# Kernel optimization log

Measured on AMD Instinct MI355X. Metric: run time of the kernel, lower is better.

Reference implementation:

```python
import jax, jax.numpy as jnp
import numpy as np

N = 50000      # nodes
E = 800000     # edges (before self-loops)
D = 128        # input_dim == hidden_dim
L = 3          # num_layers
EPS = 1e-5     # BatchNorm eps


def setup_inputs() -> dict:
    key = jax.random.key(0)
    k0, k1, k2 = jax.random.split(key, 3)
    x = jax.random.normal(k0, (N, D), dtype=jnp.float32)
    edge_index = jax.random.randint(k1, (2, E), 0, N, dtype=jnp.int32)
    # stacked per-layer params (layer 0 is input_dim->hidden, same shape since D==hidden)
    W = jax.random.normal(k2, (L, D, D), dtype=jnp.float32) / np.float32(np.sqrt(D))
    b = jnp.zeros((L, D), dtype=jnp.float32)
    gamma = jnp.ones((L, D), dtype=jnp.float32)
    beta = jnp.zeros((L, D), dtype=jnp.float32)
    return {"x": x, "edge_index": edge_index, "W": W, "b": b, "gamma": gamma, "beta": beta}


def reference(x, edge_index, W, b, gamma, beta):
    # --- GCN symmetric normalization with self-loops (PyG GCNConv default) ---
    loop = jnp.arange(N, dtype=edge_index.dtype)
    src = jnp.concatenate([edge_index[0], loop])      # [E+N]
    dst = jnp.concatenate([edge_index[1], loop])      # [E+N]
    deg = jax.ops.segment_sum(jnp.ones_like(dst, dtype=x.dtype), dst, num_segments=N)
    dinv = jax.lax.rsqrt(deg)                          # deg >= 1 due to self-loops
    norm = (dinv[src] * dinv[dst])[:, None]            # [E+N, 1]

    h = x
    for i in range(L):
        # GCNConv: aggregate norm * (h W)[src] into dst, then bias
        m = h @ W[i]                                   # [N, D]
        h = jax.ops.segment_sum(m[src] * norm, dst, num_segments=N) + b[i]
        # BatchNorm1d (training-mode batch statistics, biased variance)
        mu = jnp.mean(h, axis=0)
        var = jnp.var(h, axis=0)
        h = gamma[i] * (h - mu) * jax.lax.rsqrt(var + EPS) + beta[i]
        # ReLU; dropout is identity in eval mode
        h = jax.nn.relu(h)
    return h
```

## Files before the change

kernel.cpp:

```cpp
#include <hip/hip_runtime.h>
#include <hip/hip_bf16.h>

#define N_NODES 50000
#define N_EDGES 800000
#define DIM 128
#define BN_EPS 1e-5f
#define GATHER_BLOCKS (N_NODES / 4)
#define RED_BLOCKS 125
#define CAP 48

typedef __attribute__((ext_vector_type(8))) short short8;
typedef __attribute__((ext_vector_type(4))) float float4v;

__device__ __forceinline__ float bf16_bits_to_f32(unsigned short u) {
    union { unsigned int i; float f; } c;
    c.i = ((unsigned int)u) << 16;
    return c.f;
}

__device__ __forceinline__ float bf16_lo(unsigned int u) {
    union { unsigned int i; float f; } c;
    c.i = u << 16;
    return c.f;
}

__device__ __forceinline__ float bf16_hi(unsigned int u) {
    union { unsigned int i; float f; } c;
    c.i = u & 0xFFFF0000u;
    return c.f;
}

__device__ __forceinline__ unsigned short f32_to_bf16_bits(float f) {
    union { float f; unsigned int i; } c;
    c.f = f;
    unsigned int lsb = (c.i >> 16) & 1u;
    c.i += 0x7FFFu + lsb;
    return (unsigned short)(c.i >> 16);
}

__global__ __launch_bounds__(256) void sniff(const unsigned short* __restrict__ xu,
                                             float* __restrict__ mode) {
    __shared__ int cnt;
    if (threadIdx.x == 0) cnt = 0;
    __syncthreads();
    int ok = 0;
    for (int i = threadIdx.x; i < 512; i += 256) {
        unsigned e = (xu[i] >> 7) & 0xFFu;
        if (e >= 96u && e <= 159u) ok++;
    }
    atomicAdd(&cnt, ok);
    __syncthreads();
    if (threadIdx.x == 0) mode[0] = (cnt >= 480) ? 0.0f : 1.0f;
}

__global__ __launch_bounds__(256) void zero_buf(float* __restrict__ p, int n) {
    int i = blockIdx.x * blockDim.x + threadIdx.x;
    if (i < n) p[i] = 0.0f;
}

__global__ __launch_bounds__(256) void zero_int(int* __restrict__ p, int n) {
    int i = blockIdx.x * blockDim.x + threadIdx.x;
    if (i < n) p[i] = 0;
}

__global__ __launch_bounds__(256) void convert_params(
    const void* __restrict__ W, const void* __restrict__ b,
    const void* __restrict__ g, const void* __restrict__ be,
    const float* __restrict__ mode,
    unsigned short* __restrict__ Wt, float* __restrict__ pf32) {
    const bool mf32 = mode[0] > 0.5f;
    int i = blockIdx.x * blockDim.x + threadIdx.x;
    const int NW = 3 * DIM * DIM;
    if (i < NW) {
        int l = i >> 14;
        int rem = i & 16383;
        int k = rem >> 7;
        int n = rem & 127;
        unsigned short v = mf32 ? f32_to_bf16_bits(((const float*)W)[i])
                                : ((const unsigned short*)W)[i];
        Wt[(size_t)l * DIM * DIM + (size_t)n * DIM + k] = v;
    } else if (i < NW + 3 * 3 * DIM) {
        int p = i - NW;
        int which = p / 384;
        int r = p - which * 384;
        const void* srcp = (which == 0) ? b : (which == 1) ? g : be;
        float v = mf32 ? ((const float*)srcp)[r]
                       : bf16_bits_to_f32(((const unsigned short*)srcp)[r]);
        pf32[which * 384 + r] = v;
    }
}

__global__ __launch_bounds__(256) void fill_padded(
    const int* __restrict__ src, const int* __restrict__ dst,
    int* __restrict__ cnt, unsigned short* __restrict__ colu) {
    int e = blockIdx.x * blockDim.x + threadIdx.x;
    if (e >= N_EDGES) return;
    int s = src[e], d = dst[e];
    int pos = atomicAdd(&cnt[d], 1);
    if (pos < CAP) colu[(size_t)d * CAP + pos] = (unsigned short)s;
}

__global__ __launch_bounds__(256) void make_dinv(const int* __restrict__ cnt,
                                                 float* __restrict__ dinv) {
    int v = blockIdx.x * blockDim.x + threadIdx.x;
    if (v < N_NODES) dinv[v] = rsqrtf((float)cnt[v] + 1.0f);
}

__global__ __launch_bounds__(256) void gemm_scale(
    const void* hsrc, int kind, int b_bf16,
    const unsigned short* __restrict__ Wt,
    const float* __restrict__ dinv,
    const float* __restrict__ mode,
    const float* __restrict__ alpha, const float* __restrict__ delta,
    unsigned short* A, float* __restrict__ B, int write_b) {
    const int wave = threadIdx.x >> 6;
    const int lane = threadIdx.x & 63;
    const int quad = lane >> 4;
    const int nidx = lane & 15;
    const int row0 = blockIdx.x * 16;

    short8 afrag[4];
    if (kind == 0) {
        if (mode[0] > 0.5f) {
            const float* xf = (const float*)hsrc;
            #pragma unroll
            for (int kk = 0; kk < 4; ++kk) {
                const float4v* xr = (const float4v*)(xf + (size_t)(row0 + nidx) * DIM + kk * 32 + quad * 8);
                float4v p0 = xr[0], p1 = xr[1];
                #pragma unroll
                for (int j = 0; j < 4; ++j) {
                    afrag[kk][j]     = (short)f32_to_bf16_bits(p0[j]);
                    afrag[kk][4 + j] = (short)f32_to_bf16_bits(p1[j]);
                }
            }
        } else {
            const unsigned short* hu = (const unsigned short*)hsrc;
            #pragma unroll
            for (int kk = 0; kk < 4; ++kk)
                afrag[kk] = *(const short8*)(hu + (size_t)(row0 + nidx) * DIM + kk * 32 + quad * 8);
        }
    } else if (b_bf16) {
        const unsigned short* Bh = (const unsigned short*)hsrc;
        const float dv = dinv[row0 + nidx];
        #pragma unroll
        for (int kk = 0; kk < 4; ++kk) {
            short8 braw = *(const short8*)(Bh + (size_t)(row0 + nidx) * DIM + kk * 32 + quad * 8);
            const float* ap = alpha + kk * 32 + quad * 8;
            const float* dp = delta + kk * 32 + quad * 8;
            float4v A0 = *(const float4v*)ap, A1 = *(const float4v*)(ap + 4);
            float4v D0 = *(const float4v*)dp, D1 = *(const float4v*)(dp + 4);
            #pragma unroll
            for (int j = 0; j < 4; ++j) {
                float v0 = bf16_bits_to_f32((unsigned short)braw[j]);
                float v1 = bf16_bits_to_f32((unsigned short)braw[4 + j]);
                float h0 = fmaxf(fmaf(A0[j] * dv, v0, D0[j]), 0.f);
                float h1 = fmaxf(fmaf(A1[j] * dv, v1, D1[j]), 0.f);
                afrag[kk][j]     = (short)f32_to_bf16_bits(h0);
                afrag[kk][4 + j] = (short)f32_to_bf16_bits(h1);
            }
        }
    } else {
        const float* Bf = (const float*)hsrc;
        const float dv = dinv[row0 + nidx];
        #pragma unroll
        for (int kk = 0; kk < 4; ++kk) {
            const float* bp = Bf + (size_t)(row0 + nidx) * DIM + kk * 32 + quad * 8;
            float4v p0 = *(const float4v*)bp;
            float4v p1 = *(const float4v*)(bp + 4);
            const float* ap = alpha + kk * 32 + quad * 8;
            const float* dp = delta + kk * 32 + quad * 8;
            float4v A0 = *(const float4v*)ap, A1 = *(const float4v*)(ap + 4);
            float4v D0 = *(const float4v*)dp, D1 = *(const float4v*)(dp + 4);
            #pragma unroll
            for (int j = 0; j < 4; ++j) {
                float h0 = fmaxf(fmaf(A0[j] * dv, p0[j], D0[j]), 0.f);
                float h1 = fmaxf(fmaf(A1[j] * dv, p1[j], D1[j]), 0.f);
                afrag[kk][j]     = (short)f32_to_bf16_bits(h0);
                afrag[kk][4 + j] = (short)f32_to_bf16_bits(h1);
            }
        }
    }

    short8 bfrag[2][4];
    #pragma unroll
    for (int half = 0; half < 2; ++half) {
        int c = wave * 32 + half * 16 + nidx;
        #pragma unroll
        for (int kk = 0; kk < 4; ++kk)
            bfrag[half][kk] = *(const short8*)(Wt + (size_t)c * DIM + kk * 32 + quad * 8);
    }

    float4v acc0 = {0.f, 0.f, 0.f, 0.f};
    float4v acc1 = {0.f, 0.f, 0.f, 0.f};
    #pragma unroll
    for (int kk = 0; kk < 4; ++kk) {
        acc0 = __builtin_amdgcn_mfma_f32_16x16x32_bf16(afrag[kk], bfrag[0][kk], acc0, 0, 0, 0);
        acc1 = __builtin_amdgcn_mfma_f32_16x16x32_bf16(afrag[kk], bfrag[1][kk], acc1, 0, 0, 0);
    }

    #pragma unroll
    for (int r = 0; r < 4; ++r) {
        int row = row0 + quad * 4 + r;
        float d = dinv[row];
        float v0 = acc0[r] * d;
        float v1 = acc1[r] * d;
        size_t i0 = (size_t)row * DIM + wave * 32 + nidx;
        size_t i1 = i0 + 16;
        A[i0] = f32_to_bf16_bits(v0);
        A[i1] = f32_to_bf16_bits(v1);
        if (write_b) { B[i0] = v0; B[i1] = v1; }
    }
}

__global__ __launch_bounds__(256) void gather_csr(
    const int* __restrict__ cnt, const unsigned short* __restrict__ colu,
    const unsigned short* __restrict__ A,
    const float* __restrict__ dinv, const float* __restrict__ bias,
    unsigned short* __restrict__ Bh, float* __restrict__ partial) {
    __shared__ float sacc[4][128], sacc2[4][128];
    const int wave = threadIdx.x >> 6;
    const int lane = threadIdx.x & 63;
    const int half = lane >> 5;
    const int lid  = lane & 31;
    const int cbase = lid * 4;
    const int node = blockIdx.x * 4 + wave;
    const int lo = node * CAP;
    const int hi = lo + min(cnt[node], CAP);

    float a0 = 0.f, a1 = 0.f, a2 = 0.f, a3 = 0.f;
    if (half == 0) {
        uint2 su = *(const uint2*)(A + (size_t)node * DIM + cbase);
        a0 = bf16_lo(su.x); a1 = bf16_hi(su.x);
        a2 = bf16_lo(su.y); a3 = bf16_hi(su.y);
    }

    int e = lo + half;
    for (; e + 14 < hi; e += 16) {
        int s0 = colu[e];      int s1 = colu[e + 2];
        int s2 = colu[e + 4];  int s3 = colu[e + 6];
        int s4 = colu[e + 8];  int s5 = colu[e + 10];
        int s6 = colu[e + 12]; int s7 = colu[e + 14];
        uint2 v0 = *(const uint2*)(A + (size_t)s0 * DIM + cbase);
        uint2 v1 = *(const uint2*)(A + (size_t)s1 * DIM + cbase);
        uint2 v2 = *(const uint2*)(A + (size_t)s2 * DIM + cbase);
        uint2 v3 = *(const uint2*)(A + (size_t)s3 * DIM + cbase);
        uint2 v4 = *(const uint2*)(A + (size_t)s4 * DIM + cbase);
        uint2 v5 = *(const uint2*)(A + (size_t)s5 * DIM + cbase);
        uint2 v6 = *(const uint2*)(A + (size_t)s6 * DIM + cbase);
        uint2 v7 = *(const uint2*)(A + (size_t)s7 * DIM + cbase);
        a0 += bf16_lo(v0.x); a1 += bf16_hi(v0.x); a2 += bf16_lo(v0.y); a3 += bf16_hi(v0.y);
        a0 += bf16_lo(v1.x); a1 += bf16_hi(v1.x); a2 += bf16_lo(v1.y); a3 += bf16_hi(v1.y);
        a0 += bf16_lo(v2.x); a1 += bf16_hi(v2.x); a2 += bf16_lo(v2.y); a3 += bf16_hi(v2.y);
        a0 += bf16_lo(v3.x); a1 += bf16_hi(v3.x); a2 += bf16_lo(v3.y); a3 += bf16_hi(v3.y);
        a0 += bf16_lo(v4.x); a1 += bf16_hi(v4.x); a2 += bf16_lo(v4.y); a3 += bf16_hi(v4.y);
        a0 += bf16_lo(v5.x); a1 += bf16_hi(v5.x); a2 += bf16_lo(v5.y); a3 += bf16_hi(v5.y);
        a0 += bf16_lo(v6.x); a1 += bf16_hi(v6.x); a2 += bf16_lo(v6.y); a3 += bf16_hi(v6.y);
        a0 += bf16_lo(v7.x); a1 += bf16_hi(v7.x); a2 += bf16_lo(v7.y); a3 += bf16_hi(v7.y);
    }
    for (; e + 6 < hi; e += 8) {
        int s0 = colu[e];     int s1 = colu[e + 2];
        int s2 = colu[e + 4]; int s3 = colu[e + 6];
        uint2 v0 = *(const uint2*)(A + (size_t)s0 * DIM + cbase);
        uint2 v1 = *(const uint2*)(A + (size_t)s1 * DIM + cbase);
        uint2 v2 = *(const uint2*)(A + (size_t)s2 * DIM + cbase);
        uint2 v3 = *(const uint2*)(A + (size_t)s3 * DIM + cbase);
        a0 += bf16_lo(v0.x); a1 += bf16_hi(v0.x); a2 += bf16_lo(v0.y); a3 += bf16_hi(v0.y);
        a0 += bf16_lo(v1.x); a1 += bf16_hi(v1.x); a2 += bf16_lo(v1.y); a3 += bf16_hi(v1.y);
        a0 += bf16_lo(v2.x); a1 += bf16_hi(v2.x); a2 += bf16_lo(v2.y); a3 += bf16_hi(v2.y);
        a0 += bf16_lo(v3.x); a1 += bf16_hi(v3.x); a2 += bf16_lo(v3.y); a3 += bf16_hi(v3.y);
    }
    for (; e < hi; e += 2) {
        int s0 = colu[e];
        uint2 v0 = *(const uint2*)(A + (size_t)s0 * DIM + cbase);
        a0 += bf16_lo(v0.x); a1 += bf16_hi(v0.x);
        a2 += bf16_lo(v0.y); a3 += bf16_hi(v0.y);
    }

    a0 += __shfl_xor(a0, 32);
    a1 += __shfl_xor(a1, 32);
    a2 += __shfl_xor(a2, 32);
    a3 += __shfl_xor(a3, 32);

    if (half == 0) {
        unsigned int px = (unsigned int)f32_to_bf16_bits(a0) |
                          ((unsigned int)f32_to_bf16_bits(a1) << 16);
        unsigned int py = (unsigned int)f32_to_bf16_bits(a2) |
                          ((unsigned int)f32_to_bf16_bits(a3) << 16);
        uint2 st = {px, py};
        *(uint2*)(Bh + (size_t)node * DIM + cbase) = st;
        float4 bb = *(const float4*)(bias + cbase);
        float dv = dinv[node];
        float v0 = fmaf(dv, a0, bb.x);
        float v1 = fmaf(dv, a1, bb.y);
        float v2 = fmaf(dv, a2, bb.z);
        float v3 = fmaf(dv, a3, bb.w);
        sacc[wave][cbase]     = v0;  sacc2[wave][cbase]     = v0 * v0;
        sacc[wave][cbase + 1] = v1;  sacc2[wave][cbase + 1] = v1 * v1;
        sacc[wave][cbase + 2] = v2;  sacc2[wave][cbase + 2] = v2 * v2;
        sacc[wave][cbase + 3] = v3;  sacc2[wave][cbase + 3] = v3 * v3;
    }
    __syncthreads();
    const int t = threadIdx.x;
    float s;
    if (t < 128) s = sacc[0][t] + sacc[1][t] + sacc[2][t] + sacc[3][t];
    else { int c = t - 128; s = sacc2[0][c] + sacc2[1][c] + sacc2[2][c] + sacc2[3][c]; }
    partial[(size_t)blockIdx.x * 256 + t] = s;
}

__global__ __launch_bounds__(256) void reduce_partials(
    const float* __restrict__ partial, float* __restrict__ stats) {
    const int t = threadIdx.x;
    const int rows = GATHER_BLOCKS / RED_BLOCKS;
    const int r0 = blockIdx.x * rows;
    float s = 0.f;
    for (int i = 0; i < rows; ++i)
        s += partial[(size_t)(r0 + i) * 256 + t];
    atomicAdd(&stats[t], s);
}

__global__ __launch_bounds__(128) void bn_coefs(
    const float* __restrict__ pf32, int l,
    float* __restrict__ colsum, float* __restrict__ colsumsq,
    float* __restrict__ alpha, float* __restrict__ delta) {
    int c = threadIdx.x;
    const float invN = 1.0f / N_NODES;
    float mu = colsum[c] * invN;
    float var = colsumsq[c] * invN - mu * mu;
    float istd = rsqrtf(var + BN_EPS);
    float gg = pf32[384 + l * 128 + c];
    float bt = pf32[768 + l * 128 + c];
    float bi = pf32[l * 128 + c];
    float al = gg * istd;
    alpha[c] = al;
    delta[c] = al * (bi - mu) + bt;
    colsum[c] = 0.f;
    colsumsq[c] = 0.f;
}

__global__ __launch_bounds__(256) void hist_dst(const int* __restrict__ dst,
                                                int* __restrict__ cnt) {
    int e = blockIdx.x * blockDim.x + threadIdx.x;
    if (e < N_EDGES) atomicAdd(&cnt[dst[e]], 1);
}

__global__ __launch_bounds__(256) void scatter_edges(
    const int* __restrict__ src, const int* __restrict__ dst,
    const unsigned short* __restrict__ A, float* __restrict__ B) {
    int t = blockIdx.x * blockDim.x + threadIdx.x;
    int e = t >> 4;
    if (e >= N_EDGES) return;
    int f = (t & 15) * 8;
    int s = src[e], d = dst[e];
    short8 v = *(const short8*)(A + (size_t)s * DIM + f);
    float* bp = B + (size_t)d * DIM + f;
    #pragma unroll
    for (int j = 0; j < 8; ++j)
        atomicAdd(bp + j, bf16_bits_to_f32((unsigned short)v[j]));
}

__global__ __launch_bounds__(256) void bn_reduce(
    const float* __restrict__ B, const float* __restrict__ dinv,
    const float* __restrict__ bias,
    float* __restrict__ colsum, float* __restrict__ colsumsq) {
    int c = threadIdx.x & 127;
    int half = threadIdx.x >> 7;
    float bb = bias[c];
    float s = 0.f, s2 = 0.f;
    for (int row = blockIdx.x * 2 + half; row < N_NODES; row += gridDim.x * 2) {
        float v = dinv[row] * B[(size_t)row * DIM + c] + bb;
        s += v;
        s2 += v * v;
    }
    __shared__ float ls[128], ls2[128];
    if (half == 1) { ls[c] = s; ls2[c] = s2; }
    __syncthreads();
    if (half == 0) {
        atomicAdd(&colsum[c], s + ls[c]);
        atomicAdd(&colsumsq[c], s2 + ls2[c]);
    }
}

__global__ __launch_bounds__(256) void bn_apply(
    const void* __restrict__ Bv, int b_bf16,
    const float* __restrict__ dinv,
    const float* __restrict__ alpha, const float* __restrict__ delta,
    const float* __restrict__ mode, void* __restrict__ out) {
    int t = blockIdx.x * blockDim.x + threadIdx.x;
    if (t >= N_NODES * DIM) return;
    int row = t >> 7, c = t & 127;
    float bval = b_bf16 ? bf16_bits_to_f32(((const unsigned short*)Bv)[t])
                        : ((const float*)Bv)[t];
    float r = fmaxf(fmaf(alpha[c] * dinv[row], bval, delta[c]), 0.f);
    if (mode[0] > 0.5f)
        ((float*)out)[t] = r;
    else
        ((unsigned short*)out)[t] = f32_to_bf16_bits(r);
}

extern "C" void kernel_launch(void* const* d_in, const int* in_sizes, int n_in,
                              void* d_out, int out_size, void* d_ws, size_t ws_size,
                              hipStream_t stream) {
    const void* x  = d_in[0];
    const int*  ei = (const int*)d_in[1];
    const void* W  = d_in[2];
    const void* b  = d_in[3];
    const void* g  = d_in[4];
    const void* be = d_in[5];

    unsigned short* hA = (unsigned short*)d_out;

    char* ws = (char*)d_ws;
    size_t off = 0;
    auto alloc = [&](size_t bytes) {
        char* p = ws + off;
        off = (off + bytes + 255) & ~(size_t)255;
        return p;
    };
    float* dinv     = (float*)alloc((size_t)N_NODES * 4);
    float* B        = (float*)alloc((size_t)N_NODES * DIM * 4);
    unsigned short* Wt = (unsigned short*)alloc((size_t)3 * DIM * DIM * 2);
    float* pf32     = (float*)alloc(3 * 3 * DIM * 4);
    float* stats    = (float*)alloc(256 * 4);
    float* alphaB   = (float*)alloc(128 * 4);
    float* deltaB   = (float*)alloc(128 * 4);
    float* mode     = (float*)alloc(64 * 4);
    int*   cnt      = (int*)alloc((size_t)N_NODES * 4);
    unsigned short* colu = (unsigned short*)alloc((size_t)N_NODES * CAP * 2);
    float* partial  = (float*)alloc((size_t)GATHER_BLOCKS * 256 * 4);
    const bool csr_ok = (ws_size >= off) || (ws_size == 0);
    float* colsum = stats;
    float* colsumsq = stats + 128;
    unsigned short* Bh = (unsigned short*)B;

    const int* srcv = ei;
    const int* dstv = ei + N_EDGES;

    sniff<<<1, 256, 0, stream>>>((const unsigned short*)x, mode);
    convert_params<<<(3 * DIM * DIM + 3 * 3 * DIM + 255) / 256, 256, 0, stream>>>(
        W, b, g, be, mode, Wt, pf32);
    zero_int<<<(N_NODES + 255) / 256, 256, 0, stream>>>(cnt, N_NODES);
    zero_buf<<<1, 256, 0, stream>>>(stats, 256);
    if (csr_ok) {
        fill_padded<<<(N_EDGES + 255) / 256, 256, 0, stream>>>(srcv, dstv, cnt, colu);
    } else {
        hist_dst<<<(N_EDGES + 255) / 256, 256, 0, stream>>>(dstv, cnt);
    }
    make_dinv<<<(N_NODES + 255) / 256, 256, 0, stream>>>(cnt, dinv);

    for (int l = 0; l < 3; ++l) {
        const void* hin = (l == 0) ? x : (const void*)B;
        gemm_scale<<<N_NODES / 16, 256, 0, stream>>>(
            hin, (l == 0) ? 0 : 2, csr_ok ? 1 : 0, Wt + (size_t)l * DIM * DIM, dinv, mode,
            alphaB, deltaB, hA, B, csr_ok ? 0 : 1);
        if (csr_ok) {
            gather_csr<<<GATHER_BLOCKS, 256, 0, stream>>>(
                cnt, colu, hA, dinv, pf32 + l * 128, Bh, partial);
            reduce_partials<<<RED_BLOCKS, 256, 0, stream>>>(partial, stats);
        } else {
            scatter_edges<<<(N_EDGES * 16) / 256, 256, 0, stream>>>(srcv, dstv, hA, B);
            bn_reduce<<<256, 256, 0, stream>>>(B, dinv, pf32 + l * 128, colsum, colsumsq);
        }
        bn_coefs<<<1, 128, 0, stream>>>(pf32, l, colsum, colsumsq, alphaB, deltaB);
        if (l == 2)
            bn_apply<<<(N_NODES * DIM) / 256, 256, 0, stream>>>(
                (const void*)B, csr_ok ? 1 : 0, dinv, alphaB, deltaB, mode, d_out);
    }
}
```

Baseline: 378.1 us.

## Fuse edge bucketing with layer-0 GEMM and build CSR per partition in shared memory

Replaces the global-atomic padded-CSR fill with a two-pass scheme. Edges are first bucketed into per-partition queues, inside the same launch that runs the layer-0 GEMM. A per-partition kernel then builds the padded adjacency with shared-memory atomics and also produces the counts and dinv. Because layer-0 GEMM now runs before dinv exists, the layer-0 gather applies the source dinv weight per edge. This removes the zero_int/make_dinv launches and scattered global atomics, and overlaps graph preprocessing with the first GEMM. In exchange it adds per-edge dinv loads in layer 0 and a queue-capacity limit (QCAP) that could silently drop edges on skewed graphs.

```diff
diff --git a/kernel.cpp b/kernel.cpp
--- a/kernel.cpp
+++ b/kernel.cpp
@@ -8,6 +8,14 @@
 #define GATHER_BLOCKS (N_NODES / 4)
 #define RED_BLOCKS 125
 #define CAP 48
+
+#define PART_SHIFT 7
+#define PART_SIZE 128
+#define NPARTS ((N_NODES + PART_SIZE - 1) / PART_SIZE)
+#define NSUB 8
+#define QCAP 512
+#define FA_BLOCKS (N_EDGES / 256)
+#define GEMM_BLOCKS (N_NODES / 16)
 
 typedef __attribute__((ext_vector_type(8))) short short8;
 typedef __attribute__((ext_vector_type(4))) float float4v;
@@ -61,6 +69,12 @@
 __global__ __launch_bounds__(256) void zero_int(int* __restrict__ p, int n) {
     int i = blockIdx.x * blockDim.x + threadIdx.x;
     if (i < n) p[i] = 0;
+}
+
+__global__ __launch_bounds__(256) void zero_aux(int* __restrict__ qcnt,
+                                                float* __restrict__ stats) {
+    for (int i = threadIdx.x; i < NSUB * NPARTS; i += 256) qcnt[i] = 0;
+    stats[threadIdx.x] = 0.0f;
 }
 
 __global__ __launch_bounds__(256) void convert_params(
@@ -90,14 +104,111 @@
     }
 }
 
-__global__ __launch_bounds__(256) void fill_padded(
+__global__ __launch_bounds__(256) void fused_a(
     const int* __restrict__ src, const int* __restrict__ dst,
-    int* __restrict__ cnt, unsigned short* __restrict__ colu) {
-    int e = blockIdx.x * blockDim.x + threadIdx.x;
-    if (e >= N_EDGES) return;
-    int s = src[e], d = dst[e];
-    int pos = atomicAdd(&cnt[d], 1);
-    if (pos < CAP) colu[(size_t)d * CAP + pos] = (unsigned short)s;
+    int* __restrict__ qcnt, unsigned int* __restrict__ queue,
+    const void* __restrict__ x, const unsigned short* __restrict__ Wt,
+    const float* __restrict__ mode, unsigned short* __restrict__ A) {
+    const int bid = blockIdx.x;
+    if (bid < FA_BLOCKS) {
+        const int e = bid * 256 + threadIdx.x;
+        if (e < N_EDGES) {
+            const int d = dst[e];
+            const int s = src[e];
+            if ((unsigned)d < (unsigned)N_NODES) {
+                const int qi = (bid & (NSUB - 1)) * NPARTS + (d >> PART_SHIFT);
+                const int pos = atomicAdd(&qcnt[qi], 1);
+                if (pos < QCAP)
+                    queue[(size_t)qi * QCAP + pos] =
+                        (unsigned int)s | ((unsigned int)(d & (PART_SIZE - 1)) << 16);
+            }
+        }
+        return;
+    }
+    const int wave = threadIdx.x >> 6;
+    const int lane = threadIdx.x & 63;
+    const int quad = lane >> 4;
+    const int nidx = lane & 15;
+    const int row0 = (bid - FA_BLOCKS) * 16;
+
+    short8 afrag[4];
+    if (mode[0] > 0.5f) {
+        const float* xf = (const float*)x;
+        #pragma unroll
+        for (int kk = 0; kk < 4; ++kk) {
+            const float4v* xr = (const float4v*)(xf + (size_t)(row0 + nidx) * DIM + kk * 32 + quad * 8);
+            float4v p0 = xr[0], p1 = xr[1];
+            #pragma unroll
+            for (int j = 0; j < 4; ++j) {
+                afrag[kk][j]     = (short)f32_to_bf16_bits(p0[j]);
+                afrag[kk][4 + j] = (short)f32_to_bf16_bits(p1[j]);
+            }
+        }
+    } else {
+        const unsigned short* hu = (const unsigned short*)x;
+        #pragma unroll
+        for (int kk = 0; kk < 4; ++kk)
+            afrag[kk] = *(const short8*)(hu + (size_t)(row0 + nidx) * DIM + kk * 32 + quad * 8);
+    }
+
+    short8 bfrag[2][4];
+    #pragma unroll
+    for (int half = 0; half < 2; ++half) {
+        int c = wave * 32 + half * 16 + nidx;
+        #pragma unroll
+        for (int kk = 0; kk < 4; ++kk)
+            bfrag[half][kk] = *(const short8*)(Wt + (size_t)c * DIM + kk * 32 + quad * 8);
+    }
+
+    float4v acc0 = {0.f, 0.f, 0.f, 0.f};
+    float4v acc1 = {0.f, 0.f, 0.f, 0.f};
+    #pragma unroll
+    for (int kk = 0; kk < 4; ++kk) {
+        acc0 = __builtin_amdgcn_mfma_f32_16x16x32_bf16(afrag[kk], bfrag[0][kk], acc0, 0, 0, 0);
+        acc1 = __builtin_amdgcn_mfma_f32_16x16x32_bf16(afrag[kk], bfrag[1][kk], acc1, 0, 0, 0);
+    }
+
+    #pragma unroll
+    for (int r = 0; r < 4; ++r) {
+        int row = row0 + quad * 4 + r;
+        size_t i0 = (size_t)row * DIM + wave * 32 + nidx;
+        A[i0]      = f32_to_bf16_bits(acc0[r]);
+        A[i0 + 16] = f32_to_bf16_bits(acc1[r]);
+    }
+}
+
+__global__ __launch_bounds__(256) void csr_build(
+    const int* __restrict__ qcnt, const unsigned int* __restrict__ queue,
+    unsigned short* __restrict__ colu, int* __restrict__ cnt,
+    float* __restrict__ dinv) {
+    __shared__ int lcnt[PART_SIZE];
+    const int p = blockIdx.x;
+    if (threadIdx.x < PART_SIZE) lcnt[threadIdx.x] = 0;
+    __syncthreads();
+    const int base = p << PART_SHIFT;
+    #pragma unroll
+    for (int sub = 0; sub < NSUB; ++sub) {
+        const int qi = sub * NPARTS + p;
+        const int n = min(qcnt[qi], QCAP);
+        const unsigned int* qp = queue + (size_t)qi * QCAP;
+        for (int i = threadIdx.x; i < n; i += 256) {
+            unsigned int pk = qp[i];
+            int dl = pk >> 16;
+            int s  = pk & 0xFFFFu;
+            int pos = atomicAdd(&lcnt[dl], 1);
+            if (pos < CAP)
+                colu[(size_t)(base + dl) * CAP + pos] = (unsigned short)s;
+        }
+    }
+    __syncthreads();
+    if (threadIdx.x < PART_SIZE) {
+        int d = base + threadIdx.x;
+        if (d < N_NODES) {
+            int c = lcnt[threadIdx.x];
+            cnt[d] = c;
+            dinv[d] = rsqrtf((float)c + 1.0f);
+        }
+    }
 }
 
 __global__ __launch_bounds__(256) void make_dinv(const int* __restrict__ cnt,
@@ -212,6 +323,13 @@
     }
 }
 
+#define ACC4(v, w) do { \
+    if (SC) { a0 = fmaf(w, bf16_lo(v.x), a0); a1 = fmaf(w, bf16_hi(v.x), a1); \
+              a2 = fmaf(w, bf16_lo(v.y), a2); a3 = fmaf(w, bf16_hi(v.y), a3); } \
+    else { a0 += bf16_lo(v.x); a1 += bf16_hi(v.x); \
+           a2 += bf16_lo(v.y); a3 += bf16_hi(v.y); } } while (0)
+
+template <int SC>
 __global__ __launch_bounds__(256) void gather_csr(
     const int* __restrict__ cnt, const unsigned short* __restrict__ colu,
     const unsigned short* __restrict__ A,
@@ -226,12 +344,14 @@
     const int node = blockIdx.x * 4 + wave;
     const int lo = node * CAP;
     const int hi = lo + min(cnt[node], CAP);
+    const float dv = dinv[node];
 
     float a0 = 0.f, a1 = 0.f, a2 = 0.f, a3 = 0.f;
     if (half == 0) {
         uint2 su = *(const uint2*)(A + (size_t)node * DIM + cbase);
-        a0 = bf16_lo(su.x); a1 = bf16_hi(su.x);
-        a2 = bf16_lo(su.y); a3 = bf16_hi(su.y);
+        const float scl = SC ? dv : 1.0f;
+        a0 = scl * bf16_lo(su.x); a1 = scl * bf16_hi(su.x);
+        a2 = scl * bf16_lo(su.y); a3 = scl * bf16_hi(su.y);
     }
 
     int e = lo + half;
@@ -240,6 +360,10 @@
         int s2 = colu[e + 4];  int s3 = colu[e + 6];
         int s4 = colu[e + 8];  int s5 = colu[e + 10];
         int s6 = colu[e + 12]; int s7 = colu[e + 14];
+        float w0 = SC ? dinv[s0] : 0.f; float w1 = SC ? dinv[s1] : 0.f;
+        float w2 = SC ? dinv[s2] : 0.f; float w3 = SC ? dinv[s3] : 0.f;
+        float w4 = SC ? dinv[s4] : 0.f; float w5 = SC ? dinv[s5] : 0.f;
+        float w6 = SC ? dinv[s6] : 0.f; float w7 = SC ? dinv[s7] : 0.f;
         uint2 v0 = *(const uint2*)(A + (size_t)s0 * DIM + cbase);
         uint2 v1 = *(const uint2*)(A + (size_t)s1 * DIM + cbase);
         uint2 v2 = *(const uint2*)(A + (size_t)s2 * DIM + cbase);
@@ -248,32 +372,25 @@
         uint2 v5 = *(const uint2*)(A + (size_t)s5 * DIM + cbase);
         uint2 v6 = *(const uint2*)(A + (size_t)s6 * DIM + cbase);
         uint2 v7 = *(const uint2*)(A + (size_t)s7 * DIM + cbase);
-        a0 += bf16_lo(v0.x); a1 += bf16_hi(v0.x); a2 += bf16_lo(v0.y); a3 += bf16_hi(v0.y);
-        a0 += bf16_lo(v1.x); a1 += bf16_hi(v1.x); a2 += bf16_lo(v1.y); a3 += bf16_hi(v1.y);
-        a0 += bf16_lo(v2.x); a1 += bf16_hi(v2.x); a2 += bf16_lo(v2.y); a3 += bf16_hi(v2.y);
-        a0 += bf16_lo(v3.x); a1 += bf16_hi(v3.x); a2 += bf16_lo(v3.y); a3 += bf16_hi(v3.y);
-        a0 += bf16_lo(v4.x); a1 += bf16_hi(v4.x); a2 += bf16_lo(v4.y); a3 += bf16_hi(v4.y);
-        a0 += bf16_lo(v5.x); a1 += bf16_hi(v5.x); a2 += bf16_lo(v5.y); a3 += bf16_hi(v5.y);
-        a0 += bf16_lo(v6.x); a1 += bf16_hi(v6.x); a2 += bf16_lo(v6.y); a3 += bf16_hi(v6.y);
-        a0 += bf16_lo(v7.x); a1 += bf16_hi(v7.x); a2 += bf16_lo(v7.y); a3 += bf16_hi(v7.y);
+        ACC4(v0, w0); ACC4(v1, w1); ACC4(v2, w2); ACC4(v3, w3);
+        ACC4(v4, w4); ACC4(v5, w5); ACC4(v6, w6); ACC4(v7, w7);
     }
     for (; e + 6 < hi; e += 8) {
         int s0 = colu[e];     int s1 = colu[e + 2];
         int s2 = colu[e + 4]; int s3 = colu[e + 6];
+        float w0 = SC ? dinv[s0] : 0.f; float w1 = SC ? dinv[s1] : 0.f;
+        float w2 = SC ? dinv[s2] : 0.f; float w3 = SC ? dinv[s3] : 0.f;
         uint2 v0 = *(const uint2*)(A + (size_t)s0 * DIM + cbase);
         uint2 v1 = *(const uint2*)(A + (size_t)s1 * DIM + cbase);
         uint2 v2 = *(const uint2*)(A + (size_t)s2 * DIM + cbase);
         uint2 v3 = *(const uint2*)(A + (size_t)s3 * DIM + cbase);
-        a0 += bf16_lo(v0.x); a1 += bf16_hi(v0.x); a2 += bf16_lo(v0.y); a3 += bf16_hi(v0.y);
-        a0 += bf16_lo(v1.x); a1 += bf16_hi(v1.x); a2 += bf16_lo(v1.y); a3 += bf16_hi(v1.y);
-        a0 += bf16_lo(v2.x); a1 += bf16_hi(v2.x); a2 += bf16_lo(v2.y); a3 += bf16_hi(v2.y);
-        a0 += bf16_lo(v3.x); a1 += bf16_hi(v3.x); a2 += bf16_lo(v3.y); a3 += bf16_hi(v3.y);
+        ACC4(v0, w0); ACC4(v1, w1); ACC4(v2, w2); ACC4(v3, w3);
     }
     for (; e < hi; e += 2) {
         int s0 = colu[e];
+        float w0 = SC ? dinv[s0] : 0.f;
         uint2 v0 = *(const uint2*)(A + (size_t)s0 * DIM + cbase);
-        a0 += bf16_lo(v0.x); a1 += bf16_hi(v0.x);
-        a2 += bf16_lo(v0.y); a3 += bf16_hi(v0.y);
+        ACC4(v0, w0);
     }
 
     a0 += __shfl_xor(a0, 32);
@@ -289,7 +406,6 @@
         uint2 st = {px, py};
         *(uint2*)(Bh + (size_t)node * DIM + cbase) = st;
         float4 bb = *(const float4*)(bias + cbase);
-        float dv = dinv[node];
         float v0 = fmaf(dv, a0, bb.x);
         float v1 = fmaf(dv, a1, bb.y);
         float v2 = fmaf(dv, a2, bb.z);
@@ -427,6 +543,8 @@
     int*   cnt      = (int*)alloc((size_t)N_NODES * 4);
     unsigned short* colu = (unsigned short*)alloc((size_t)N_NODES * CAP * 2);
     float* partial  = (float*)alloc((size_t)GATHER_BLOCKS * 256 * 4);
+    int*   qcnt     = (int*)alloc((size_t)NSUB * NPARTS * 4);
+    unsigned int* queue = (unsigned int*)partial;
     const bool csr_ok = (ws_size >= off) || (ws_size == 0);
     float* colsum = stats;
     float* colsumsq = stats + 128;
@@ -438,31 +556,47 @@
     sniff<<<1, 256, 0, stream>>>((const unsigned short*)x, mode);
     convert_params<<<(3 * DIM * DIM + 3 * 3 * DIM + 255) / 256, 256, 0, stream>>>(
         W, b, g, be, mode, Wt, pf32);
-    zero_int<<<(N_NODES + 255) / 256, 256, 0, stream>>>(cnt, N_NODES);
-    zero_buf<<<1, 256, 0, stream>>>(stats, 256);
+
     if (csr_ok) {
-        fill_padded<<<(N_EDGES + 255) / 256, 256, 0, stream>>>(srcv, dstv, cnt, colu);
+        zero_aux<<<1, 256, 0, stream>>>(qcnt, stats);
+        fused_a<<<FA_BLOCKS + GEMM_BLOCKS, 256, 0, stream>>>(
+            srcv, dstv, qcnt, queue, x, Wt, mode, hA);
+        csr_build<<<NPARTS, 256, 0, stream>>>(qcnt, queue, colu, cnt, dinv);
+
+        for (int l = 0; l < 3; ++l) {
+            if (l > 0)
+                gemm_scale<<<GEMM_BLOCKS, 256, 0, stream>>>(
+                    (const void*)B, 2, 1, Wt + (size_t)l * DIM * DIM, dinv, mode,
+                    alphaB, deltaB, hA, B, 0);
+            if (l == 0)
+                gather_csr<1><<<GATHER_BLOCKS, 256, 0, stream>>>(
+                    cnt, colu, hA, dinv, pf32 + l * 128, Bh, partial);
+            else
+                gather_csr<0><<<GATHER_BLOCKS, 256, 0, stream>>>(
+                    cnt, colu, hA, dinv, pf32 + l * 128, Bh, partial);
+            reduce_partials<<<RED_BLOCKS, 256, 0, stream>>>(partial, stats);
+            bn_coefs<<<1, 128, 0, stream>>>(pf32, l, colsum, colsumsq, alphaB, deltaB);
+            if (l == 2)
+                bn_apply<<<(N_NODES * DIM) / 256, 256, 0, stream>>>(
+                    (const void*)B, 1, dinv, alphaB, deltaB, mode, d_out);
+        }
     } else {
+        zero_int<<<(N_NODES + 255) / 256, 256, 0, stream>>>(cnt, N_NODES);
+        zero_buf<<<1, 256, 0, stream>>>(stats, 256);
         hist_dst<<<(N_EDGES + 255) / 256, 256, 0, stream>>>(dstv, cnt);
-    }
-    make_dinv<<<(N_NODES + 255) / 256, 256, 0, stream>>>(cnt, dinv);
-
-    for (int l = 0; l < 3; ++l) {
-        const void* hin = (l == 0) ? x : (const void*)B;
-        gemm_scale<<<N_NODES / 16, 256, 0, stream>>>(
-            hin, (l == 0) ? 0 : 2, csr_ok ? 1 : 0, Wt + (size_t)l * DIM * DIM, dinv, mode,
-            alphaB, deltaB, hA, B, csr_ok ? 0 : 1);
-        if (csr_ok) {
-            gather_csr<<<GATHER_BLOCKS, 256, 0, stream>>>(
-                cnt, colu, hA, dinv, pf32 + l * 128, Bh, partial);
-            reduce_partials<<<RED_BLOCKS, 256, 0, stream>>>(partial, stats);
-        } else {
+        make_dinv<<<(N_NODES + 255) / 256, 256, 0, stream>>>(cnt, dinv);
+
+        for (int l = 0; l < 3; ++l) {
+            const void* hin = (l == 0) ? x : (const void*)B;
+            gemm_scale<<<GEMM_BLOCKS, 256, 0, stream>>>(
+                hin, (l == 0) ? 0 : 2, 0, Wt + (size_t)l * DIM * DIM, dinv, mode,
+                alphaB, deltaB, hA, B, 1);
             scatter_edges<<<(N_EDGES * 16) / 256, 256, 0, stream>>>(srcv, dstv, hA, B);
             bn_reduce<<<256, 256, 0, stream>>>(B, dinv, pf32 + l * 128, colsum, colsumsq);
-        }
-        bn_coefs<<<1, 128, 0, stream>>>(pf32, l, colsum, colsumsq, alphaB, deltaB);
-        if (l == 2)
-            bn_apply<<<(N_NODES * DIM) / 256, 256, 0, stream>>>(
-                (const void*)B, csr_ok ? 1 : 0, dinv, alphaB, deltaB, mode, d_out);
-    }
-}
+            bn_coefs<<<1, 128, 0, stream>>>(pf32, l, colsum, colsumsq, alphaB, deltaB);
+            if (l == 2)
+                bn_apply<<<(N_NODES * DIM) / 256, 256, 0, stream>>>(
+                    (const void*)B, 0, dinv, alphaB, deltaB, mode, d_out);
+        }
+    }
+}
```

Result: slower. 401.6 us (+6.2%).
